# Kernel optimization log

Hardware: AMD Instinct MI355X
Metric: run time of the kernel (lower is better)

Reference implementation:

```python
import jax, jax.numpy as jnp
import numpy as np

# dims
N, Lx, Ff = 2048, 168, 64          # batch, encoder seq len, encoder features
HID = 256                           # GRU hidden size
Ly, Ft, FOUT, BINS = 72, 22, 10, 8  # decoder steps, future feats, output size, rain classes
DEC_IN = Ft + FOUT                  # 32, GRUCell input = cat(y_t, p)
REG_H, CLS_H = 128, 128             # head hidden widths
BETA = 1.1                          # SmeLU beta


def smelu(x):
    # SmeLU: 0 for x<=-b, x for x>=b, (x+b)^2/(4b) in between
    return jnp.where(x >= BETA, x,
                     jnp.where(x <= -BETA, jnp.zeros_like(x),
                               (x + BETA) ** 2 / (4.0 * BETA)))


def gru_step(h, u, Wih, Whh, bih, bhh):
    # torch GRU/GRUCell gate math; Wih: (3H, in), Whh: (3H, H)
    gi = u @ Wih.T + bih
    gh = h @ Whh.T + bhh
    i_r, i_z, i_n = jnp.split(gi, 3, axis=-1)
    h_r, h_z, h_n = jnp.split(gh, 3, axis=-1)
    r = jax.nn.sigmoid(i_r + h_r)
    z = jax.nn.sigmoid(i_z + h_z)
    n = jnp.tanh(i_n + r * h_n)
    return (1.0 - z) * n + z * h


def setup_inputs() -> dict:
    key = jax.random.key(0)
    ks = jax.random.split(key, 24)
    s = 1.0 / np.sqrt(HID)

    def rn(k, shape, scale):
        return jax.random.normal(k, shape, dtype=jnp.float32) * scale

    return {
        'x_f': rn(ks[0], (N, Lx, Ff), 1.0),
        'x': rn(ks[1], (N, Lx, FOUT), 1.0),      # unused by forward (matches torch)
        'y_t': rn(ks[2], (N, Ly + 1, Ft), 1.0),
        'p': rn(ks[3], (N, Ly + 1, FOUT), 1.0),
        # encoder GRU (1 layer, unidirectional)
        'enc_Wih': rn(ks[4], (3 * HID, Ff), s), 'enc_Whh': rn(ks[5], (3 * HID, HID), s),
        'enc_bih': rn(ks[6], (3 * HID,), s), 'enc_bhh': rn(ks[7], (3 * HID,), s),
        # decoder GRUCell
        'dec_Wih': rn(ks[8], (3 * HID, DEC_IN), s), 'dec_Whh': rn(ks[9], (3 * HID, HID), s),
        'dec_bih': rn(ks[10], (3 * HID,), s), 'dec_bhh': rn(ks[11], (3 * HID,), s),
        # temphr head: HID -> REG_H -> (FOUT - BINS)
        'th_W0': rn(ks[12], (REG_H, HID), s), 'th_b0': rn(ks[13], (REG_H,), s),
        'th_W1': rn(ks[14], (FOUT - BINS, REG_H), 1.0 / np.sqrt(REG_H)), 'th_b1': rn(ks[15], (FOUT - BINS,), 0.05),
        # class head: HID -> CLS_H -> BINS
        'cl_W0': rn(ks[16], (CLS_H, HID), s), 'cl_b0': rn(ks[17], (CLS_H,), s),
        'cl_W1': rn(ks[18], (BINS, CLS_H), 1.0 / np.sqrt(CLS_H)), 'cl_b1': rn(ks[19], (BINS,), 0.05),
    }


def reference(x_f, x, y_t, p,
              enc_Wih, enc_Whh, enc_bih, enc_bhh,
              dec_Wih, dec_Whh, dec_bih, dec_bhh,
              th_W0, th_b0, th_W1, th_b1,
              cl_W0, cl_b0, cl_W1, cl_b1):
    # ---- encoder: run GRU over Lx, keep final hidden (N, HID) ----
    h0 = jnp.zeros((x_f.shape[0], HID), dtype=x_f.dtype)
    enc_xs = jnp.swapaxes(x_f, 0, 1)  # (Lx, N, Ff)

    def enc_body(h, u):
        return gru_step(h, u, enc_Wih, enc_Whh, enc_bih, enc_bhh), None

    h_enc, _ = jax.lax.scan(enc_body, h0, enc_xs)

    # ---- decoder inputs: torch loop uses cat(y_t,p) at index 0, then i-1 ----
    ytp = jnp.concatenate([y_t[:, :-1, :], p[:, :-1, :]], axis=-1)  # (N, Ly, DEC_IN)
    idx = jnp.concatenate([jnp.zeros((1,), jnp.int32), jnp.arange(Ly - 1, dtype=jnp.int32)])
    dec_in = jnp.swapaxes(ytp[:, idx, :], 0, 1)  # (Ly, N, DEC_IN)

    def dec_body(h, u):
        h2 = gru_step(h, u, dec_Wih, dec_Whh, dec_bih, dec_bhh)
        th = smelu(h2 @ th_W0.T + th_b0) @ th_W1.T + th_b1   # (N, 2)
        cl = smelu(h2 @ cl_W0.T + cl_b0) @ cl_W1.T + cl_b1   # (N, BINS)
        return h2, jnp.concatenate([th, cl], axis=-1)

    _, outs = jax.lax.scan(dec_body, h_enc, dec_in)  # (Ly, N, FOUT)
    return jnp.swapaxes(outs, 0, 1)  # (N, Ly, FOUT)
```

## Files before the change

kernel.cpp:

```cpp
#include <hip/hip_runtime.h>

typedef __bf16 v8bf __attribute__((ext_vector_type(8)));
typedef float v4f __attribute__((ext_vector_type(4)));
typedef float v4ff __attribute__((ext_vector_type(4)));
typedef unsigned short u16;
typedef unsigned int u32;

#define DEVI __device__ __forceinline__

constexpr int LX = 168, FF = 64;
constexpr int LY = 72, FT = 22, FOUTC = 10;
constexpr int HID = 256;
constexpr int HSTR = 264;
constexpr int UST2 = 40;
constexpr int A1STR = 264;
constexpr int SSTR = 264;

constexpr int W_EWIH = 0;
constexpr int W_EWHH = 49152;
constexpr int W_DWIH = 245760;
constexpr int W_DWHH = 270336;
constexpr int W_THW0 = 466944;
constexpr int W_THW1 = 499712;
constexpr int W_CLW0 = 499968;
constexpr int W_CLW1 = 532736;
constexpr int W_TOTAL = 533760;

DEVI u16 f2bf(float f) {
  u32 x; __builtin_memcpy(&x, &f, 4);
  return (u16)((x + 0x7FFFu + ((x >> 16) & 1u)) >> 16);
}
DEVI float sigm(float x) { return __builtin_amdgcn_rcpf(1.f + __expf(-x)); }
DEVI float tanh_(float x) {
  float e = __expf(-2.f * fabsf(x));
  return copysignf((1.f - e) * __builtin_amdgcn_rcpf(1.f + e), x);
}
DEVI float smelu_(float x) {
  if (x >= 1.1f) return x;
  if (x <= -1.1f) return 0.f;
  float u = x + 1.1f;
  return u * u * (1.f / 4.4f);
}
DEVI v8bf ld8(const u16* p) { return *reinterpret_cast<const v8bf*>(p); }
DEVI v4f ldw(const u16* p) { return *reinterpret_cast<const v4f*>(p); }
DEVI v8bf asbf(v4f x) { return __builtin_bit_cast(v8bf, x); }
DEVI void pin(v4f& x) { asm("" : "+v"(x)); }
DEVI void pinf(v4ff& x) { asm("" : "+v"(x)); }
DEVI v4f mfma16(v8bf a, v8bf b, v4f c) {
  return __builtin_amdgcn_mfma_f32_16x16x32_bf16(a, b, c, 0, 0, 0);
}
DEVI v8bf cvt2f(v4ff lo, v4ff hi) {
  v8bf r;
#pragma unroll
  for (int j = 0; j < 4; ++j) { r[j] = (__bf16)lo[j]; r[4 + j] = (__bf16)hi[j]; }
  return r;
}

__global__ void cvt_weights(const float* __restrict__ eWih, const float* __restrict__ eWhh,
                            const float* __restrict__ dWih, const float* __restrict__ dWhh,
                            const float* __restrict__ thW0, const float* __restrict__ thW1,
                            const float* __restrict__ clW0, const float* __restrict__ clW1,
                            u16* __restrict__ ws) {
  const int i = blockIdx.x * 256 + threadIdx.x;
  if (i >= W_TOTAL) return;
  const float* src; int off;
  if      (i < W_EWHH) { src = eWih; off = W_EWIH; }
  else if (i < W_DWIH) { src = eWhh; off = W_EWHH; }
  else if (i < W_DWHH) { src = dWih; off = W_DWIH; }
  else if (i < W_THW0) { src = dWhh; off = W_DWHH; }
  else if (i < W_THW1) { src = thW0; off = W_THW0; }
  else if (i < W_CLW0) { src = thW1; off = W_THW1; }
  else if (i < W_CLW1) { src = clW0; off = W_CLW0; }
  else                 { src = clW1; off = W_CLW1; }
  ws[i] = f2bf(src[i - off]);
}

__global__ __launch_bounds__(512, 2) void encdec_kernel(
    const float* __restrict__ xf, const float* __restrict__ yt, const float* __restrict__ pp,
    const float* __restrict__ ebih, const float* __restrict__ ebhh,
    const float* __restrict__ dbih, const float* __restrict__ dbhh,
    const float* __restrict__ thb0, const float* __restrict__ thb1,
    const float* __restrict__ clb0, const float* __restrict__ clb1,
    const u16* __restrict__ ws, float* __restrict__ outp) {
  __shared__ __align__(16) u16 slab[256 * SSTR];
  __shared__ __align__(16) u16 hls[2][16 * HSTR];
  __shared__ __align__(16) u16 uls[2][16 * UST2];
  __shared__ __align__(16) u16 a1buf[16 * A1STR];

  const u16* eWih = ws + W_EWIH;
  const u16* eWhh = ws + W_EWHH;
  const u16* dWih = ws + W_DWIH;
  const u16* dWhh = ws + W_DWHH;
  const u16* thW0 = ws + W_THW0;
  const u16* thW1 = ws + W_THW1;
  const u16* clW0 = ws + W_CLW0;
  const u16* clW1 = ws + W_CLW1;

  const int tid = threadIdx.x;
  const int wave = tid >> 6;
  const int lane = tid & 63;
  const int col16 = lane & 15;
  const int quad = lane >> 4;
  const int n0 = blockIdx.x * 16;

  for (int i = tid; i < 16 * HSTR; i += 512) hls[0][i] = 0;

  float hreg[2][4];
#pragma unroll
  for (int j = 0; j < 2; ++j)
#pragma unroll
    for (int r = 0; r < 4; ++r) hreg[j][r] = 0.f;

  v4f wz[2][8], wn[2][8];
  v4f wiz[2][2];
  float bsr[2], bsz[2], bin_[2], bhn[2];

  {
    for (int i = tid; i < 256 * 32; i += 512) {
      const int row = i >> 5, kb = (i & 31) << 3;
      *reinterpret_cast<v8bf*>(&slab[row * SSTR + kb]) = ld8(eWhh + row * HID + kb);
    }
#pragma unroll
    for (int j = 0; j < 2; ++j) {
      const int c = wave + 8 * j;
      const int mr = c * 16 + col16, mz = 256 + mr, mn = 512 + mr;
#pragma unroll
      for (int k = 0; k < 8; ++k) {
        wz[j][k] = ldw(eWhh + (size_t)mz * HID + k * 32 + quad * 8); pin(wz[j][k]);
        wn[j][k] = ldw(eWhh + (size_t)mn * HID + k * 32 + quad * 8); pin(wn[j][k]);
      }
      wiz[j][0] = ldw(eWih + (size_t)mz * FF + quad * 8);      pin(wiz[j][0]);
      wiz[j][1] = ldw(eWih + (size_t)mz * FF + 32 + quad * 8); pin(wiz[j][1]);
      bsr[j] = ebih[mr] + ebhh[mr];
      bsz[j] = ebih[mz] + ebhh[mz];
      bin_[j] = ebih[mn];
      bhn[j] = ebhh[mn];
    }
    const float* xbase = xf + (size_t)(n0 + col16) * LX * FF + quad * 8;
    v4ff xr0 = *(const v4ff*)(xbase);
    v4ff xr1 = *(const v4ff*)(xbase + 4);
    v4ff xr2 = *(const v4ff*)(xbase + 32);
    v4ff xr3 = *(const v4ff*)(xbase + 36);
    __syncthreads();

#pragma unroll 1
    for (int t = 0; t < LX; ++t) {
      v4ff xn0, xn1, xn2, xn3;
      if (t + 1 < LX) {
        const float* xn = xbase + (size_t)(t + 1) * FF;
        xn0 = *(const v4ff*)(xn);      pinf(xn0);
        xn1 = *(const v4ff*)(xn + 4);  pinf(xn1);
        xn2 = *(const v4ff*)(xn + 32); pinf(xn2);
        xn3 = *(const v4ff*)(xn + 36); pinf(xn3);
      }
      const u16* hb = hls[t & 1] + col16 * HSTR + quad * 8;
      v8bf a[8];
#pragma unroll
      for (int k = 0; k < 8; ++k) a[k] = ld8(hb + k * 32);
      const v8bf xa0 = cvt2f(xr0, xr1);
      const v8bf xa1 = cvt2f(xr2, xr3);

      float zg[2][4];
#pragma unroll
      for (int j = 0; j < 2; ++j) {
        v4f acc = {0.f, 0.f, 0.f, 0.f};
#pragma unroll
        for (int k = 0; k < 8; ++k) acc = mfma16(a[k], asbf(wz[j][k]), acc);
        acc = mfma16(xa0, asbf(wiz[j][0]), acc);
        acc = mfma16(xa1, asbf(wiz[j][1]), acc);
#pragma unroll
        for (int r = 0; r < 4; ++r) zg[j][r] = sigm(acc[r] + bsz[j]);
      }
      float rg[2][4];
#pragma unroll
      for (int j = 0; j < 2; ++j) {
        const int c = wave + 8 * j;
        const u16* pw = eWih + (size_t)(c * 16 + col16) * FF + quad * 8;
        const v8bf wir0 = ld8(pw), wir1 = ld8(pw + 32);
        const u16* sp = slab + (c * 16 + col16) * SSTR + quad * 8;
        v4f acc = {0.f, 0.f, 0.f, 0.f};
#pragma unroll
        for (int k = 0; k < 8; ++k) acc = mfma16(a[k], ld8(sp + k * 32), acc);
        acc = mfma16(xa0, wir0, acc);
        acc = mfma16(xa1, wir1, acc);
#pragma unroll
        for (int r = 0; r < 4; ++r) rg[j][r] = sigm(acc[r] + bsr[j]);
      }
#pragma unroll
      for (int j = 0; j < 2; ++j) {
        const int c = wave + 8 * j;
        const u16* pw = eWih + (size_t)(512 + c * 16 + col16) * FF + quad * 8;
        const v8bf win0 = ld8(pw), win1 = ld8(pw + 32);
        v4f ah = {0.f, 0.f, 0.f, 0.f};
#pragma unroll
        for (int k = 0; k < 8; ++k) ah = mfma16(a[k], asbf(wn[j][k]), ah);
        v4f ai = {0.f, 0.f, 0.f, 0.f};
        ai = mfma16(xa0, win0, ai);
        ai = mfma16(xa1, win1, ai);
        const int cidx = c * 16 + col16;
#pragma unroll
        for (int r = 0; r < 4; ++r) {
          const float ng = tanh_(ai[r] + bin_[j] + rg[j][r] * (ah[r] + bhn[j]));
          hreg[j][r] = (1.f - zg[j][r]) * ng + zg[j][r] * hreg[j][r];
          hls[(t + 1) & 1][(quad * 4 + r) * HSTR + cidx] = f2bf(hreg[j][r]);
        }
      }
      __syncthreads();
      xr0 = xn0; xr1 = xn1; xr2 = xn2; xr3 = xn3;
    }
  }

  {
    for (int i = tid; i < 256 * 32; i += 512) {
      const int row = i >> 5, kb = (i & 31) << 3;
      *reinterpret_cast<v8bf*>(&slab[row * SSTR + kb]) = ld8(dWhh + row * HID + kb);
    }
    float hb0[2];
#pragma unroll
    for (int j = 0; j < 2; ++j) {
      const int c = wave + 8 * j;
      const int mr = c * 16 + col16, mz = 256 + mr, mn = 512 + mr;
#pragma unroll
      for (int k = 0; k < 8; ++k) {
        wz[j][k] = ldw(dWhh + (size_t)mz * HID + k * 32 + quad * 8); pin(wz[j][k]);
        wn[j][k] = ldw(dWhh + (size_t)mn * HID + k * 32 + quad * 8); pin(wn[j][k]);
      }
      wiz[j][0] = ldw(dWih + (size_t)mz * 32 + quad * 8); pin(wiz[j][0]);
      bsr[j] = dbih[mr] + dbhh[mr];
      bsz[j] = dbih[mz] + dbhh[mz];
      bin_[j] = dbih[mn];
      bhn[j] = dbhh[mn];
      const int ml = wave * 16 + col16;
      hb0[j] = (j == 0) ? thb0[ml] : clb0[ml];
    }
    const bool w1th = (col16 < 2);
    const bool w1cl = (col16 >= 2 && col16 < FOUTC);
    const float b1v = w1th ? thb1[col16] : (w1cl ? clb1[col16 - 2] : 0.f);

    {
      const int rr = tid >> 5, cc = tid & 31;
      const size_t yb = (size_t)(n0 + rr) * (LY + 1);
      const float v = (cc < FT) ? yt[yb * FT + cc] : pp[yb * FOUTC + (cc - FT)];
      uls[0][rr * UST2 + cc] = f2bf(v);
    }
    __syncthreads();

    const int srr = tid >> 5, scc = tid & 31;
    const size_t ybase = (size_t)(n0 + srr) * (LY + 1);

#pragma unroll 1
    for (int t = 0; t < LY; ++t) {
      float un = 0.f;
      if (t + 1 < LY)
        un = (scc < FT) ? yt[(ybase + t) * FT + scc]
                        : pp[(ybase + t) * FOUTC + (scc - FT)];
      const v8bf ua = ld8(uls[t & 1] + col16 * UST2 + quad * 8);
      const u16* hb = hls[t & 1] + col16 * HSTR + quad * 8;
      v8bf a[8];
#pragma unroll
      for (int k = 0; k < 8; ++k) a[k] = ld8(hb + k * 32);

      float zg[2][4];
#pragma unroll
      for (int j = 0; j < 2; ++j) {
        v4f acc = {0.f, 0.f, 0.f, 0.f};
#pragma unroll
        for (int k = 0; k < 8; ++k) acc = mfma16(a[k], asbf(wz[j][k]), acc);
        acc = mfma16(ua, asbf(wiz[j][0]), acc);
#pragma unroll
        for (int r = 0; r < 4; ++r) zg[j][r] = sigm(acc[r] + bsz[j]);
      }
      float rg[2][4];
#pragma unroll
      for (int j = 0; j < 2; ++j) {
        const int c = wave + 8 * j;
        const v8bf wir0 = ld8(dWih + (size_t)(c * 16 + col16) * 32 + quad * 8);
        const u16* sp = slab + (c * 16 + col16) * SSTR + quad * 8;
        v4f acc = {0.f, 0.f, 0.f, 0.f};
#pragma unroll
        for (int k = 0; k < 8; ++k) acc = mfma16(a[k], ld8(sp + k * 32), acc);
        acc = mfma16(ua, wir0, acc);
#pragma unroll
        for (int r = 0; r < 4; ++r) rg[j][r] = sigm(acc[r] + bsr[j]);
      }
#pragma unroll
      for (int j = 0; j < 2; ++j) {
        const int c = wave + 8 * j;
        const v8bf win0 = ld8(dWih + (size_t)(512 + c * 16 + col16) * 32 + quad * 8);
        v4f ah = {0.f, 0.f, 0.f, 0.f};
#pragma unroll
        for (int k = 0; k < 8; ++k) ah = mfma16(a[k], asbf(wn[j][k]), ah);
        v4f ai = {0.f, 0.f, 0.f, 0.f};
        ai = mfma16(ua, win0, ai);
        const int cidx = c * 16 + col16;
#pragma unroll
        for (int r = 0; r < 4; ++r) {
          const float ng = tanh_(ai[r] + bin_[j] + rg[j][r] * (ah[r] + bhn[j]));
          hreg[j][r] = (1.f - zg[j][r]) * ng + zg[j][r] * hreg[j][r];
          hls[(t + 1) & 1][(quad * 4 + r) * HSTR + cidx] = f2bf(hreg[j][r]);
        }
      }
      if (t + 1 < LY) uls[(t + 1) & 1][srr * UST2 + scc] = f2bf(un);
      __syncthreads();

      {
        v8bf w0f[2][8];
        const u16* pw0 = thW0 + (size_t)(wave * 16 + col16) * HID + quad * 8;
        const u16* pw1 = clW0 + (size_t)(wave * 16 + col16) * HID + quad * 8;
#pragma unroll
        for (int k = 0; k < 8; ++k) {
          w0f[0][k] = ld8(pw0 + k * 32);
          w0f[1][k] = ld8(pw1 + k * 32);
        }
        const u16* h2b = hls[(t + 1) & 1] + col16 * HSTR + quad * 8;
        v8bf ah2[8];
#pragma unroll
        for (int k = 0; k < 8; ++k) ah2[k] = ld8(h2b + k * 32);
#pragma unroll
        for (int j = 0; j < 2; ++j) {
          const int c = wave + 8 * j;
          v4f acc = {0.f, 0.f, 0.f, 0.f};
#pragma unroll
          for (int k = 0; k < 8; ++k) acc = mfma16(ah2[k], w0f[j][k], acc);
#pragma unroll
          for (int r = 0; r < 4; ++r)
            a1buf[(quad * 4 + r) * A1STR + c * 16 + col16] =
                f2bf(smelu_(acc[r] + hb0[j]));
        }
      }
      __syncthreads();

      if (wave == 0) {
        const u16* arow = a1buf + col16 * A1STR + quad * 8;
        v4f acc = {0.f, 0.f, 0.f, 0.f};
#pragma unroll
        for (int kt = 0; kt < 8; ++kt) {
          v8bf b;
#pragma unroll
          for (int j = 0; j < 8; ++j) b[j] = (__bf16)0.0f;
          if (kt < 4) {
            if (w1th) b = ld8(thW1 + col16 * 128 + kt * 32 + quad * 8);
          } else {
            if (w1cl) b = ld8(clW1 + (col16 - 2) * 128 + (kt - 4) * 32 + quad * 8);
          }
          acc = mfma16(ld8(arow + kt * 32), b, acc);
        }
        if (col16 < FOUTC) {
#pragma unroll
          for (int r = 0; r < 4; ++r)
            outp[((size_t)(n0 + quad * 4 + r) * LY + t) * FOUTC + col16] =
                acc[r] + b1v;
        }
      }
    }
  }
}

extern "C" void kernel_launch(void* const* d_in, const int* in_sizes, int n_in,
                              void* d_out, int out_size, void* d_ws, size_t ws_size,
                              hipStream_t stream) {
  (void)in_sizes; (void)n_in; (void)ws_size; (void)out_size;
  const float* xf   = (const float*)d_in[0];
  const float* yt   = (const float*)d_in[2];
  const float* pp   = (const float*)d_in[3];
  const float* eWih = (const float*)d_in[4];
  const float* eWhh = (const float*)d_in[5];
  const float* ebih = (const float*)d_in[6];
  const float* ebhh = (const float*)d_in[7];
  const float* dWih = (const float*)d_in[8];
  const float* dWhh = (const float*)d_in[9];
  const float* dbih = (const float*)d_in[10];
  const float* dbhh = (const float*)d_in[11];
  const float* thW0 = (const float*)d_in[12];
  const float* thb0 = (const float*)d_in[13];
  const float* thW1 = (const float*)d_in[14];
  const float* thb1 = (const float*)d_in[15];
  const float* clW0 = (const float*)d_in[16];
  const float* clb0 = (const float*)d_in[17];
  const float* clW1 = (const float*)d_in[18];
  const float* clb1 = (const float*)d_in[19];
  float* outp = (float*)d_out;
  u16* ws = (u16*)d_ws;

  cvt_weights<<<dim3((W_TOTAL + 255) / 256), dim3(256), 0, stream>>>(
      eWih, eWhh, dWih, dWhh, thW0, thW1, clW0, clW1, ws);
  encdec_kernel<<<dim3(128), dim3(512), 0, stream>>>(
      xf, yt, pp, ebih, ebhh, dbih, dbhh, thb0, thb1, clb0, clb1, ws, outp);
}
```

Measured before the change: 1.464 ms.

## Software-pipeline decoder heads across steps and interleave GRU gate MFMA chains

The decoder loop now runs the output heads one and two steps behind the recurrence. The first head layer reuses the h fragments already loaded for the next GRU step, and the second layer reads a double-buffered activation tile, which drops one barrier per step. The hidden state becomes single-buffered, with a barrier after each read. In both encoder and decoder the six gate accumulators are interleaved across k to give independent MFMA chains, and the register-pinned input-weight z fragments are replaced by per-step global loads. This trades fewer barriers and more MFMA ILP against extra global weight loads and a more complex epilogue.

```diff
diff --git a/kernel.cpp b/kernel.cpp
--- a/kernel.cpp
+++ b/kernel.cpp
@@ -13,7 +13,6 @@
 constexpr int HID = 256;
 constexpr int HSTR = 264;
 constexpr int UST2 = 40;
-constexpr int A1STR = 264;
 constexpr int SSTR = 264;
 
 constexpr int W_EWIH = 0;
@@ -45,7 +44,6 @@
 DEVI v4f ldw(const u16* p) { return *reinterpret_cast<const v4f*>(p); }
 DEVI v8bf asbf(v4f x) { return __builtin_bit_cast(v8bf, x); }
 DEVI void pin(v4f& x) { asm("" : "+v"(x)); }
-DEVI void pinf(v4ff& x) { asm("" : "+v"(x)); }
 DEVI v4f mfma16(v8bf a, v8bf b, v4f c) {
   return __builtin_amdgcn_mfma_f32_16x16x32_bf16(a, b, c, 0, 0, 0);
 }
@@ -84,8 +82,8 @@
     const u16* __restrict__ ws, float* __restrict__ outp) {
   __shared__ __align__(16) u16 slab[256 * SSTR];
   __shared__ __align__(16) u16 hls[2][16 * HSTR];
+  __shared__ __align__(16) u16 a1x[16 * HSTR];
   __shared__ __align__(16) u16 uls[2][16 * UST2];
-  __shared__ __align__(16) u16 a1buf[16 * A1STR];
 
   const u16* eWih = ws + W_EWIH;
   const u16* eWhh = ws + W_EWHH;
@@ -112,7 +110,6 @@
     for (int r = 0; r < 4; ++r) hreg[j][r] = 0.f;
 
   v4f wz[2][8], wn[2][8];
-  v4f wiz[2][2];
   float bsr[2], bsz[2], bin_[2], bhn[2];
 
   {
@@ -129,84 +126,69 @@
         wz[j][k] = ldw(eWhh + (size_t)mz * HID + k * 32 + quad * 8); pin(wz[j][k]);
         wn[j][k] = ldw(eWhh + (size_t)mn * HID + k * 32 + quad * 8); pin(wn[j][k]);
       }
-      wiz[j][0] = ldw(eWih + (size_t)mz * FF + quad * 8);      pin(wiz[j][0]);
-      wiz[j][1] = ldw(eWih + (size_t)mz * FF + 32 + quad * 8); pin(wiz[j][1]);
       bsr[j] = ebih[mr] + ebhh[mr];
       bsz[j] = ebih[mz] + ebhh[mz];
       bin_[j] = ebih[mn];
       bhn[j] = ebhh[mn];
     }
     const float* xbase = xf + (size_t)(n0 + col16) * LX * FF + quad * 8;
-    v4ff xr0 = *(const v4ff*)(xbase);
-    v4ff xr1 = *(const v4ff*)(xbase + 4);
-    v4ff xr2 = *(const v4ff*)(xbase + 32);
-    v4ff xr3 = *(const v4ff*)(xbase + 36);
+    const u16* sp0 = slab + (wave * 16 + col16) * SSTR + quad * 8;
+    const u16* sp1 = slab + ((wave + 8) * 16 + col16) * SSTR + quad * 8;
     __syncthreads();
 
 #pragma unroll 1
     for (int t = 0; t < LX; ++t) {
-      v4ff xn0, xn1, xn2, xn3;
-      if (t + 1 < LX) {
-        const float* xn = xbase + (size_t)(t + 1) * FF;
-        xn0 = *(const v4ff*)(xn);      pinf(xn0);
-        xn1 = *(const v4ff*)(xn + 4);  pinf(xn1);
-        xn2 = *(const v4ff*)(xn + 32); pinf(xn2);
-        xn3 = *(const v4ff*)(xn + 36); pinf(xn3);
-      }
+      const float* xr = xbase + (size_t)t * FF;
+      const v4ff x0 = *(const v4ff*)(xr);
+      const v4ff x1 = *(const v4ff*)(xr + 4);
+      const v4ff x2 = *(const v4ff*)(xr + 32);
+      const v4ff x3 = *(const v4ff*)(xr + 36);
       const u16* hb = hls[t & 1] + col16 * HSTR + quad * 8;
       v8bf a[8];
 #pragma unroll
       for (int k = 0; k < 8; ++k) a[k] = ld8(hb + k * 32);
-      const v8bf xa0 = cvt2f(xr0, xr1);
-      const v8bf xa1 = cvt2f(xr2, xr3);
-
-      float zg[2][4];
+
+      v4f az[2] = {{0.f,0.f,0.f,0.f},{0.f,0.f,0.f,0.f}};
+      v4f ar[2] = {{0.f,0.f,0.f,0.f},{0.f,0.f,0.f,0.f}};
+      v4f an[2] = {{0.f,0.f,0.f,0.f},{0.f,0.f,0.f,0.f}};
+#pragma unroll
+      for (int k = 0; k < 8; ++k) {
+        az[0] = mfma16(a[k], asbf(wz[0][k]), az[0]);
+        az[1] = mfma16(a[k], asbf(wz[1][k]), az[1]);
+        ar[0] = mfma16(a[k], ld8(sp0 + k * 32), ar[0]);
+        ar[1] = mfma16(a[k], ld8(sp1 + k * 32), ar[1]);
+        an[0] = mfma16(a[k], asbf(wn[0][k]), an[0]);
+        an[1] = mfma16(a[k], asbf(wn[1][k]), an[1]);
+      }
+      const v8bf xa0 = cvt2f(x0, x1);
+      const v8bf xa1 = cvt2f(x2, x3);
+      v4f ai[2] = {{0.f,0.f,0.f,0.f},{0.f,0.f,0.f,0.f}};
 #pragma unroll
       for (int j = 0; j < 2; ++j) {
-        v4f acc = {0.f, 0.f, 0.f, 0.f};
-#pragma unroll
-        for (int k = 0; k < 8; ++k) acc = mfma16(a[k], asbf(wz[j][k]), acc);
-        acc = mfma16(xa0, asbf(wiz[j][0]), acc);
-        acc = mfma16(xa1, asbf(wiz[j][1]), acc);
-#pragma unroll
-        for (int r = 0; r < 4; ++r) zg[j][r] = sigm(acc[r] + bsz[j]);
-      }
-      float rg[2][4];
+        const int m = (wave + 8 * j) * 16 + col16;
+        const u16* pwr = eWih + (size_t)m * FF + quad * 8;
+        const u16* pwz = eWih + (size_t)(256 + m) * FF + quad * 8;
+        const u16* pwn = eWih + (size_t)(512 + m) * FF + quad * 8;
+        az[j] = mfma16(xa0, ld8(pwz), az[j]);
+        az[j] = mfma16(xa1, ld8(pwz + 32), az[j]);
+        ar[j] = mfma16(xa0, ld8(pwr), ar[j]);
+        ar[j] = mfma16(xa1, ld8(pwr + 32), ar[j]);
+        ai[j] = mfma16(xa0, ld8(pwn), ai[j]);
+        ai[j] = mfma16(xa1, ld8(pwn + 32), ai[j]);
+      }
 #pragma unroll
       for (int j = 0; j < 2; ++j) {
-        const int c = wave + 8 * j;
-        const u16* pw = eWih + (size_t)(c * 16 + col16) * FF + quad * 8;
-        const v8bf wir0 = ld8(pw), wir1 = ld8(pw + 32);
-        const u16* sp = slab + (c * 16 + col16) * SSTR + quad * 8;
-        v4f acc = {0.f, 0.f, 0.f, 0.f};
-#pragma unroll
-        for (int k = 0; k < 8; ++k) acc = mfma16(a[k], ld8(sp + k * 32), acc);
-        acc = mfma16(xa0, wir0, acc);
-        acc = mfma16(xa1, wir1, acc);
-#pragma unroll
-        for (int r = 0; r < 4; ++r) rg[j][r] = sigm(acc[r] + bsr[j]);
-      }
-#pragma unroll
-      for (int j = 0; j < 2; ++j) {
-        const int c = wave + 8 * j;
-        const u16* pw = eWih + (size_t)(512 + c * 16 + col16) * FF + quad * 8;
-        const v8bf win0 = ld8(pw), win1 = ld8(pw + 32);
-        v4f ah = {0.f, 0.f, 0.f, 0.f};
-#pragma unroll
-        for (int k = 0; k < 8; ++k) ah = mfma16(a[k], asbf(wn[j][k]), ah);
-        v4f ai = {0.f, 0.f, 0.f, 0.f};
-        ai = mfma16(xa0, win0, ai);
-        ai = mfma16(xa1, win1, ai);
-        const int cidx = c * 16 + col16;
+        const int cidx = (wave + 8 * j) * 16 + col16;
 #pragma unroll
         for (int r = 0; r < 4; ++r) {
-          const float ng = tanh_(ai[r] + bin_[j] + rg[j][r] * (ah[r] + bhn[j]));
-          hreg[j][r] = (1.f - zg[j][r]) * ng + zg[j][r] * hreg[j][r];
+          const float zg = sigm(az[j][r] + bsz[j]);
+          const float rg = sigm(ar[j][r] + bsr[j]);
+          const float ng = tanh_(ai[j][r] + bin_[j] + rg * (an[j][r] + bhn[j]));
+          hreg[j][r] = (1.f - zg) * ng + zg * hreg[j][r];
           hls[(t + 1) & 1][(quad * 4 + r) * HSTR + cidx] = f2bf(hreg[j][r]);
         }
       }
       __syncthreads();
-      xr0 = xn0; xr1 = xn1; xr2 = xn2; xr3 = xn3;
     }
   }
 
@@ -225,7 +207,6 @@
         wz[j][k] = ldw(dWhh + (size_t)mz * HID + k * 32 + quad * 8); pin(wz[j][k]);
         wn[j][k] = ldw(dWhh + (size_t)mn * HID + k * 32 + quad * 8); pin(wn[j][k]);
       }
-      wiz[j][0] = ldw(dWih + (size_t)mz * 32 + quad * 8); pin(wiz[j][0]);
       bsr[j] = dbih[mr] + dbhh[mr];
       bsz[j] = dbih[mz] + dbhh[mz];
       bin_[j] = dbih[mn];
@@ -236,17 +217,16 @@
     const bool w1th = (col16 < 2);
     const bool w1cl = (col16 >= 2 && col16 < FOUTC);
     const float b1v = w1th ? thb1[col16] : (w1cl ? clb1[col16 - 2] : 0.f);
-
-    {
-      const int rr = tid >> 5, cc = tid & 31;
-      const size_t yb = (size_t)(n0 + rr) * (LY + 1);
-      const float v = (cc < FT) ? yt[yb * FT + cc] : pp[yb * FOUTC + (cc - FT)];
-      uls[0][rr * UST2 + cc] = f2bf(v);
-    }
-    __syncthreads();
+    const u16* sp0 = slab + (wave * 16 + col16) * SSTR + quad * 8;
+    const u16* sp1 = slab + ((wave + 8) * 16 + col16) * SSTR + quad * 8;
 
     const int srr = tid >> 5, scc = tid & 31;
     const size_t ybase = (size_t)(n0 + srr) * (LY + 1);
+    {
+      const float v = (scc < FT) ? yt[ybase * FT + scc] : pp[ybase * FOUTC + (scc - FT)];
+      uls[0][srr * UST2 + scc] = f2bf(v);
+    }
+    __syncthreads();
 
 #pragma unroll 1
     for (int t = 0; t < LY; ++t) {
@@ -255,100 +235,140 @@
         un = (scc < FT) ? yt[(ybase + t) * FT + scc]
                         : pp[(ybase + t) * FOUTC + (scc - FT)];
       const v8bf ua = ld8(uls[t & 1] + col16 * UST2 + quad * 8);
-      const u16* hb = hls[t & 1] + col16 * HSTR + quad * 8;
+      const u16* hb = hls[0] + col16 * HSTR + quad * 8;
       v8bf a[8];
 #pragma unroll
       for (int k = 0; k < 8; ++k) a[k] = ld8(hb + k * 32);
-
-      float zg[2][4];
+      __syncthreads();
+
+      if (wave == 0 && t >= 2) {
+        const u16* arow = ((t & 1) ? a1x : hls[1]) + col16 * HSTR + quad * 8;
+        v4f acc = {0.f, 0.f, 0.f, 0.f};
+#pragma unroll
+        for (int kt = 0; kt < 8; ++kt) {
+          v8bf b;
+#pragma unroll
+          for (int j = 0; j < 8; ++j) b[j] = (__bf16)0.0f;
+          if (kt < 4) { if (w1th) b = ld8(thW1 + col16 * 128 + kt * 32 + quad * 8); }
+          else        { if (w1cl) b = ld8(clW1 + (col16 - 2) * 128 + (kt - 4) * 32 + quad * 8); }
+          acc = mfma16(ld8(arow + kt * 32), b, acc);
+        }
+        if (col16 < FOUTC) {
+#pragma unroll
+          for (int r = 0; r < 4; ++r)
+            outp[((size_t)(n0 + quad * 4 + r) * LY + (t - 2)) * FOUTC + col16] =
+                acc[r] + b1v;
+        }
+      }
+
+      v4f az[2] = {{0.f,0.f,0.f,0.f},{0.f,0.f,0.f,0.f}};
+      v4f ar[2] = {{0.f,0.f,0.f,0.f},{0.f,0.f,0.f,0.f}};
+      v4f an[2] = {{0.f,0.f,0.f,0.f},{0.f,0.f,0.f,0.f}};
+#pragma unroll
+      for (int k = 0; k < 8; ++k) {
+        az[0] = mfma16(a[k], asbf(wz[0][k]), az[0]);
+        az[1] = mfma16(a[k], asbf(wz[1][k]), az[1]);
+        ar[0] = mfma16(a[k], ld8(sp0 + k * 32), ar[0]);
+        ar[1] = mfma16(a[k], ld8(sp1 + k * 32), ar[1]);
+        an[0] = mfma16(a[k], asbf(wn[0][k]), an[0]);
+        an[1] = mfma16(a[k], asbf(wn[1][k]), an[1]);
+      }
+      v4f ai[2] = {{0.f,0.f,0.f,0.f},{0.f,0.f,0.f,0.f}};
 #pragma unroll
       for (int j = 0; j < 2; ++j) {
-        v4f acc = {0.f, 0.f, 0.f, 0.f};
-#pragma unroll
-        for (int k = 0; k < 8; ++k) acc = mfma16(a[k], asbf(wz[j][k]), acc);
-        acc = mfma16(ua, asbf(wiz[j][0]), acc);
-#pragma unroll
-        for (int r = 0; r < 4; ++r) zg[j][r] = sigm(acc[r] + bsz[j]);
-      }
-      float rg[2][4];
+        const int m = (wave + 8 * j) * 16 + col16;
+        az[j] = mfma16(ua, ld8(dWih + (size_t)(256 + m) * 32 + quad * 8), az[j]);
+        ar[j] = mfma16(ua, ld8(dWih + (size_t)m * 32 + quad * 8), ar[j]);
+        ai[j] = mfma16(ua, ld8(dWih + (size_t)(512 + m) * 32 + quad * 8), ai[j]);
+      }
 #pragma unroll
       for (int j = 0; j < 2; ++j) {
-        const int c = wave + 8 * j;
-        const v8bf wir0 = ld8(dWih + (size_t)(c * 16 + col16) * 32 + quad * 8);
-        const u16* sp = slab + (c * 16 + col16) * SSTR + quad * 8;
-        v4f acc = {0.f, 0.f, 0.f, 0.f};
-#pragma unroll
-        for (int k = 0; k < 8; ++k) acc = mfma16(a[k], ld8(sp + k * 32), acc);
-        acc = mfma16(ua, wir0, acc);
-#pragma unroll
-        for (int r = 0; r < 4; ++r) rg[j][r] = sigm(acc[r] + bsr[j]);
-      }
-#pragma unroll
-      for (int j = 0; j < 2; ++j) {
-        const int c = wave + 8 * j;
-        const v8bf win0 = ld8(dWih + (size_t)(512 + c * 16 + col16) * 32 + quad * 8);
-        v4f ah = {0.f, 0.f, 0.f, 0.f};
-#pragma unroll
-        for (int k = 0; k < 8; ++k) ah = mfma16(a[k], asbf(wn[j][k]), ah);
-        v4f ai = {0.f, 0.f, 0.f, 0.f};
-        ai = mfma16(ua, win0, ai);
-        const int cidx = c * 16 + col16;
+        const int cidx = (wave + 8 * j) * 16 + col16;
 #pragma unroll
         for (int r = 0; r < 4; ++r) {
-          const float ng = tanh_(ai[r] + bin_[j] + rg[j][r] * (ah[r] + bhn[j]));
-          hreg[j][r] = (1.f - zg[j][r]) * ng + zg[j][r] * hreg[j][r];
-          hls[(t + 1) & 1][(quad * 4 + r) * HSTR + cidx] = f2bf(hreg[j][r]);
+          const float zg = sigm(az[j][r] + bsz[j]);
+          const float rg = sigm(ar[j][r] + bsr[j]);
+          const float ng = tanh_(ai[j][r] + bin_[j] + rg * (an[j][r] + bhn[j]));
+          hreg[j][r] = (1.f - zg) * ng + zg * hreg[j][r];
+          hls[0][(quad * 4 + r) * HSTR + cidx] = f2bf(hreg[j][r]);
+        }
+      }
+
+      if (t >= 1) {
+        u16* a1w = ((t - 1) & 1) ? a1x : hls[1];
+#pragma unroll
+        for (int j = 0; j < 2; ++j) {
+          const u16* W0 = (j == 0) ? thW0 : clW0;
+          const u16* pw = W0 + (size_t)(wave * 16 + col16) * HID + quad * 8;
+          v4f acc = {0.f, 0.f, 0.f, 0.f};
+#pragma unroll
+          for (int k = 0; k < 8; ++k) acc = mfma16(a[k], ld8(pw + k * 32), acc);
+          const int c = wave + 8 * j;
+#pragma unroll
+          for (int r = 0; r < 4; ++r)
+            a1w[(quad * 4 + r) * HSTR + c * 16 + col16] =
+                f2bf(smelu_(acc[r] + hb0[j]));
         }
       }
       if (t + 1 < LY) uls[(t + 1) & 1][srr * UST2 + scc] = f2bf(un);
       __syncthreads();
-
-      {
-        v8bf w0f[2][8];
-        const u16* pw0 = thW0 + (size_t)(wave * 16 + col16) * HID + quad * 8;
-        const u16* pw1 = clW0 + (size_t)(wave * 16 + col16) * HID + quad * 8;
-#pragma unroll
-        for (int k = 0; k < 8; ++k) {
-          w0f[0][k] = ld8(pw0 + k * 32);
-          w0f[1][k] = ld8(pw1 + k * 32);
-        }
-        const u16* h2b = hls[(t + 1) & 1] + col16 * HSTR + quad * 8;
-        v8bf ah2[8];
-#pragma unroll
-        for (int k = 0; k < 8; ++k) ah2[k] = ld8(h2b + k * 32);
-#pragma unroll
-        for (int j = 0; j < 2; ++j) {
-          const int c = wave + 8 * j;
-          v4f acc = {0.f, 0.f, 0.f, 0.f};
-#pragma unroll
-          for (int k = 0; k < 8; ++k) acc = mfma16(ah2[k], w0f[j][k], acc);
-#pragma unroll
-          for (int r = 0; r < 4; ++r)
-            a1buf[(quad * 4 + r) * A1STR + c * 16 + col16] =
-                f2bf(smelu_(acc[r] + hb0[j]));
-        }
-      }
-      __syncthreads();
-
+    }
+
+    {
+      const u16* h2b = hls[0] + col16 * HSTR + quad * 8;
+      v8bf ah2[8];
+#pragma unroll
+      for (int k = 0; k < 8; ++k) ah2[k] = ld8(h2b + k * 32);
+      u16* a1w = ((LY - 1) & 1) ? a1x : hls[1];
+#pragma unroll
+      for (int j = 0; j < 2; ++j) {
+        const u16* W0 = (j == 0) ? thW0 : clW0;
+        const u16* pw = W0 + (size_t)(wave * 16 + col16) * HID + quad * 8;
+        v4f acc = {0.f, 0.f, 0.f, 0.f};
+#pragma unroll
+        for (int k = 0; k < 8; ++k) acc = mfma16(ah2[k], ld8(pw + k * 32), acc);
+        const int c = wave + 8 * j;
+#pragma unroll
+        for (int r = 0; r < 4; ++r)
+          a1w[(quad * 4 + r) * HSTR + c * 16 + col16] =
+              f2bf(smelu_(acc[r] + hb0[j]));
+      }
       if (wave == 0) {
-        const u16* arow = a1buf + col16 * A1STR + quad * 8;
+        const u16* arow = (((LY - 2) & 1) ? a1x : hls[1]) + col16 * HSTR + quad * 8;
         v4f acc = {0.f, 0.f, 0.f, 0.f};
 #pragma unroll
         for (int kt = 0; kt < 8; ++kt) {
           v8bf b;
 #pragma unroll
           for (int j = 0; j < 8; ++j) b[j] = (__bf16)0.0f;
-          if (kt < 4) {
-            if (w1th) b = ld8(thW1 + col16 * 128 + kt * 32 + quad * 8);
-          } else {
-            if (w1cl) b = ld8(clW1 + (col16 - 2) * 128 + (kt - 4) * 32 + quad * 8);
-          }
+          if (kt < 4) { if (w1th) b = ld8(thW1 + col16 * 128 + kt * 32 + quad * 8); }
+          else        { if (w1cl) b = ld8(clW1 + (col16 - 2) * 128 + (kt - 4) * 32 + quad * 8); }
           acc = mfma16(ld8(arow + kt * 32), b, acc);
         }
         if (col16 < FOUTC) {
 #pragma unroll
           for (int r = 0; r < 4; ++r)
-            outp[((size_t)(n0 + quad * 4 + r) * LY + t) * FOUTC + col16] =
+            outp[((size_t)(n0 + quad * 4 + r) * LY + (LY - 2)) * FOUTC + col16] =
+                acc[r] + b1v;
+        }
+      }
+      __syncthreads();
+      if (wave == 0) {
+        const u16* arow = (((LY - 1) & 1) ? a1x : hls[1]) + col16 * HSTR + quad * 8;
+        v4f acc = {0.f, 0.f, 0.f, 0.f};
+#pragma unroll
+        for (int kt = 0; kt < 8; ++kt) {
+          v8bf b;
+#pragma unroll
+          for (int j = 0; j < 8; ++j) b[j] = (__bf16)0.0f;
+          if (kt < 4) { if (w1th) b = ld8(thW1 + col16 * 128 + kt * 32 + quad * 8); }
+          else        { if (w1cl) b = ld8(clW1 + (col16 - 2) * 128 + (kt - 4) * 32 + quad * 8); }
+          acc = mfma16(ld8(arow + kt * 32), b, acc);
+        }
+        if (col16 < FOUTC) {
+#pragma unroll
+          for (int r = 0; r < 4; ++r)
+            outp[((size_t)(n0 + quad * 4 + r) * LY + (LY - 1)) * FOUTC + col16] =
                 acc[r] + b1v;
         }
       }
```

Result: faster. 1.179 ms (-19.5%).
